# Kernel tuning notes

Measured on AMD Instinct MI355X. Metric: run time of the kernel, lower is better.

The kernel has to match this reference:

```python
import jax, jax.numpy as jnp
import numpy as np

B, S, D = 4, 8192, 512      # batch, seq_len, dim
P, M = 32, 2048             # num_persistent_memory, memory_size
EPS = 1e-5


def setup_inputs() -> dict:
    key = jax.random.key(0)
    ks = jax.random.split(key, 8)
    s = 1.0 / np.sqrt(D)

    def lin_w(k):
        return jax.random.uniform(k, (D, D), jnp.float32, -s, s)

    return {
        "x": jax.random.normal(ks[0], (B, S, D), jnp.float32),
        "persistent_memory": jax.random.normal(ks[1], (P, D), jnp.float32),
        "Wk": lin_w(ks[2]), "bk": jnp.zeros((D,), jnp.float32),
        "Wv": lin_w(ks[3]), "bv": jnp.zeros((D,), jnp.float32),
        "Wq": lin_w(ks[4]), "bq": jnp.zeros((D,), jnp.float32),
        "gamma": jnp.ones((D,), jnp.float32),
        "beta": jnp.zeros((D,), jnp.float32),
        "Wout": lin_w(ks[5]), "bout": jnp.zeros((D,), jnp.float32),
    }


def reference(x, persistent_memory, Wk, bk, Wv, bv, Wq, bq, gamma, beta, Wout, bout):
    b = x.shape[0]
    # concat persistent tokens: [B, T, D], T = P + S
    pm = jnp.broadcast_to(persistent_memory[None], (b, P, D))
    c = jnp.concatenate([pm, x], axis=1)

    k = c @ Wk + bk
    v = c @ Wv + bv
    q = c @ Wq + bq
    scale = 1.0 / jnp.sqrt(jnp.asarray(D, c.dtype))

    # init_state -> zeros [B, M, D]
    state0 = jnp.zeros((b, M, D), c.dtype)

    # update: write combined tokens into memory slots via cross-attention
    write_attn = jax.nn.softmax(jnp.einsum('bmd,btd->bmt', state0, k) * scale, axis=-1)  # [B,M,T]
    state = state0 + jnp.einsum('bmt,btd->bmd', write_attn, v)                           # [B,M,D]

    # retrieve: read memory with projected queries
    read_attn = jax.nn.softmax(jnp.einsum('btd,bmd->btm', q, state) * scale, axis=-1)    # [B,T,M]
    mem_out = jnp.einsum('btm,bmd->btd', read_attn, state)                               # [B,T,D]

    # LayerNorm
    mu = jnp.mean(mem_out, axis=-1, keepdims=True)
    var = jnp.mean((mem_out - mu) ** 2, axis=-1, keepdims=True)
    normed = (mem_out - mu) / jnp.sqrt(var + EPS) * gamma + beta

    # output projection (dropout is identity in eval mode)
    return normed @ Wout + bout
```

## Files before the change

kernel.cpp:

```cpp
#include <hip/hip_runtime.h>
#include <math.h>

#define BB 4
#define SS 8192
#define DD 512
#define PP 32
#define TT (PP + SS)
#define EPSV 1e-5f

typedef float f4 __attribute__((ext_vector_type(4)));


__global__ __launch_bounds__(512) void k_colsum(const f4* __restrict__ x4,
                                                f4* __restrict__ part4,
                                                float* __restrict__ z,
                                                const float* __restrict__ bout) {
  const int bb    = blockIdx.x >> 8;
  const int chunk = blockIdx.x & 255;
  const int tid   = threadIdx.x;

  const f4* p = x4 + ((size_t)bb * SS + (size_t)chunk * 32) * (DD / 4);

  f4 a = {0.f, 0.f, 0.f, 0.f};
#pragma unroll
  for (int i = 0; i < 8; ++i) {
    f4 t = __builtin_nontemporal_load(&p[i * 512 + tid]);
    a += t;
  }

  __shared__ f4 sh[512];
  sh[tid] = a;
  __syncthreads();

  if (tid < 128) {
    f4 r = sh[tid] + sh[tid + 128] + sh[tid + 256] + sh[tid + 384];
    part4[blockIdx.x * 128 + tid] = r;
  }

  if (blockIdx.x < BB) z[blockIdx.x * DD + tid] = bout[tid];
}

__global__ __launch_bounds__(512) void k_vbar(const float* __restrict__ part,
                                              const float* __restrict__ pm,
                                              const float* __restrict__ Wv,
                                              float* __restrict__ vpart) {
  const int bb = blockIdx.x >> 5;
  const int ch = blockIdx.x & 31;
  const int j  = threadIdx.x;

  __shared__ float aSh[16];
  {
    const int d16  = j >> 5;
    const int lane = j & 31;
    const int col  = ch * 16 + d16;
    float s0 = 0.f, s1 = 0.f;
#pragma unroll
    for (int k = 0; k < 4; ++k) {
      s0 += part[(size_t)(bb * 256 + lane + 64 * k) * DD + col];
      s1 += part[(size_t)(bb * 256 + lane + 64 * k + 32) * DD + col];
    }
    float s = s0 + s1 + pm[lane * DD + col];
#pragma unroll
    for (int off = 16; off > 0; off >>= 1) s += __shfl_down(s, off, 32);
    if (lane == 0) aSh[d16] = s * (1.0f / (float)TT);
  }
  __syncthreads();

  float acc = 0.f;
#pragma unroll
  for (int i = 0; i < 16; ++i)
    acc += aSh[i] * Wv[(ch * 16 + i) * DD + j];
  vpart[(bb * 32 + ch) * DD + j] = acc;
}

__global__ __launch_bounds__(512) void k_zmat(const float* __restrict__ vpart,
                                              const float* __restrict__ bv,
                                              const float* __restrict__ gamma,
                                              const float* __restrict__ beta,
                                              const float* __restrict__ Wout,
                                              float* __restrict__ z) {
  const int bb = blockIdx.x >> 5;
  const int ch = blockIdx.x & 31;
  const int j  = threadIdx.x;

  float va = bv[j], vb = 0.f;
#pragma unroll
  for (int c = 0; c < 16; ++c) {
    va += vpart[(bb * 32 + c) * DD + j];
    vb += vpart[(bb * 32 + c + 16) * DD + j];
  }
  const float v = va + vb;

  float v1 = v, v2 = v * v;
#pragma unroll
  for (int off = 32; off > 0; off >>= 1) {
    v1 += __shfl_down(v1, off, 64);
    v2 += __shfl_down(v2, off, 64);
  }
  __shared__ float w1[8], w2[8];
  const int wave = j >> 6;
  if ((j & 63) == 0) { w1[wave] = v1; w2[wave] = v2; }
  __syncthreads();
  float t1 = 0.f, t2 = 0.f;
#pragma unroll
  for (int w = 0; w < 8; ++w) { t1 += w1[w]; t2 += w2[w]; }
  const float mu  = t1 * (1.0f / (float)DD);
  const float var = t2 * (1.0f / (float)DD) - mu * mu;
  const float inv = 1.0f / sqrtf(var + EPSV);

  __shared__ float y[DD];
  y[j] = (v - mu) * inv * gamma[j] + beta[j];
  __syncthreads();

  float acc = 0.f;
#pragma unroll
  for (int i = 0; i < 16; ++i)
    acc += y[ch * 16 + i] * Wout[(ch * 16 + i) * DD + j];
  atomicAdd(&z[bb * DD + j], acc);
}

__global__ __launch_bounds__(256) void k_bcast(const f4* __restrict__ z4,
                                               f4* __restrict__ out4) {
  const unsigned i  = blockIdx.x * 256u + threadIdx.x;
  const unsigned bb = i / 1052672u;
  const unsigned j4 = i & 127u;
  __builtin_nontemporal_store(z4[bb * 128u + j4], &out4[i]);
}

extern "C" void kernel_launch(void* const* d_in, const int* in_sizes, int n_in,
                              void* d_out, int out_size, void* d_ws, size_t ws_size,
                              hipStream_t stream) {
  const float* x     = (const float*)d_in[0];
  const float* pm    = (const float*)d_in[1];
  const float* Wv    = (const float*)d_in[4];
  const float* bv    = (const float*)d_in[5];
  const float* gamma = (const float*)d_in[8];
  const float* beta  = (const float*)d_in[9];
  const float* Wout  = (const float*)d_in[10];
  const float* bout  = (const float*)d_in[11];

  float* part  = (float*)d_ws;
  float* vpart = part + 1024 * DD;
  float* z     = vpart + 128 * DD;

  k_colsum<<<1024, 512, 0, stream>>>((const f4*)x, (f4*)part, z, bout);

  k_vbar<<<BB * 32, 512, 0, stream>>>(part, pm, Wv, vpart);

  k_zmat<<<BB * 32, 512, 0, stream>>>(vpart, bv, gamma, beta, Wout, z);

  const unsigned total4 = (unsigned)BB * TT * DD / 4;
  k_bcast<<<total4 / 256, 256, 0, stream>>>((const f4*)z, (f4*)d_out);
}
```

Baseline: 144.1 us.

## Fuse vbar and zmat via algebraic LayerNorm split, shrink colsum grid

Merges the two middle kernels into one by rewriting LayerNorm-then-Wout algebraically: per-batch sum and sum-of-squares are accumulated with atomics, and the normalisation is applied in the broadcast kernel as inv*(v·gamma·Wout - mu·gamma·Wout) + beta·Wout + bout. The column-sum kernel now uses 256 larger blocks plus helper blocks that sum persistent memory and zero the accumulators. Nontemporal loads and stores are dropped. This removes one launch and its dependency, but makes the broadcast kernel compute per element, and the accumulators rely on atomics whose summation order is not fixed.

```diff
diff --git a/kernel.cpp b/kernel.cpp
--- a/kernel.cpp
+++ b/kernel.cpp
@@ -11,120 +11,146 @@
 typedef float f4 __attribute__((ext_vector_type(4)));
 
 
+#define OFF_PART  0
+#define OFF_PMSUM (256 * DD)
+#define OFF_AZ    (OFF_PMSUM + DD)
+#define OFF_G     (OFF_AZ + BB * DD)
+#define OFF_BZ    (OFF_G + DD)
+#define OFF_SV    (OFF_BZ + DD)
+#define OFF_SV2   (OFF_SV + BB * 16)
+
 __global__ __launch_bounds__(512) void k_colsum(const f4* __restrict__ x4,
-                                                f4* __restrict__ part4,
-                                                float* __restrict__ z,
-                                                const float* __restrict__ bout) {
-  const int bb    = blockIdx.x >> 8;
-  const int chunk = blockIdx.x & 255;
+                                                const float* __restrict__ pm,
+                                                const float* __restrict__ bout,
+                                                float* __restrict__ ws) {
+  const int tid = threadIdx.x;
+
+  if (blockIdx.x < 256) {
+    const int bb    = blockIdx.x >> 6;
+    const int chunk = blockIdx.x & 63;
+    const f4* p = x4 + ((size_t)bb * SS + (size_t)chunk * 128) * (DD / 4);
+
+    f4 a = {0.f, 0.f, 0.f, 0.f};
+#pragma unroll 8
+    for (int i = 0; i < 32; ++i)
+      a += p[i * 512 + tid];
+
+    __shared__ f4 sh[512];
+    sh[tid] = a;
+    __syncthreads();
+    if (tid < 128) {
+      f4 r = sh[tid] + sh[tid + 128] + sh[tid + 256] + sh[tid + 384];
+      ((f4*)(ws + OFF_PART))[blockIdx.x * 128 + tid] = r;
+    }
+  } else if (blockIdx.x == 256) {
+    float s = 0.f;
+#pragma unroll
+    for (int p = 0; p < PP; ++p) s += pm[p * DD + tid];
+    ws[OFF_PMSUM + tid] = s;
+  } else {
+#pragma unroll
+    for (int k = 0; k < BB; ++k) ws[OFF_AZ + k * DD + tid] = 0.f;
+    ws[OFF_G + tid]  = 0.f;
+    ws[OFF_BZ + tid] = bout[tid];
+    if (tid < BB) { ws[OFF_SV + tid * 16] = 0.f; ws[OFF_SV2 + tid * 16] = 0.f; }
+  }
+}
+
+__global__ __launch_bounds__(512) void k_mid(const float* __restrict__ Wv,
+                                             const float* __restrict__ bv,
+                                             const float* __restrict__ gamma,
+                                             const float* __restrict__ beta,
+                                             const float* __restrict__ Wout,
+                                             float* __restrict__ ws) {
+  const int bb    = blockIdx.x >> 5;
+  const int slice = blockIdx.x & 31;
   const int tid   = threadIdx.x;
 
-  const f4* p = x4 + ((size_t)bb * SS + (size_t)chunk * 32) * (DD / 4);
+  __shared__ float cbar[DD];
+  __shared__ float red[8][16];
+  __shared__ float vgSh[16];
 
-  f4 a = {0.f, 0.f, 0.f, 0.f};
-#pragma unroll
-  for (int i = 0; i < 8; ++i) {
-    f4 t = __builtin_nontemporal_load(&p[i * 512 + tid]);
-    a += t;
-  }
-
-  __shared__ f4 sh[512];
-  sh[tid] = a;
-  __syncthreads();
-
-  if (tid < 128) {
-    f4 r = sh[tid] + sh[tid + 128] + sh[tid + 256] + sh[tid + 384];
-    part4[blockIdx.x * 128 + tid] = r;
-  }
-
-  if (blockIdx.x < BB) z[blockIdx.x * DD + tid] = bout[tid];
-}
-
-__global__ __launch_bounds__(512) void k_vbar(const float* __restrict__ part,
-                                              const float* __restrict__ pm,
-                                              const float* __restrict__ Wv,
-                                              float* __restrict__ vpart) {
-  const int bb = blockIdx.x >> 5;
-  const int ch = blockIdx.x & 31;
-  const int j  = threadIdx.x;
-
-  __shared__ float aSh[16];
   {
-    const int d16  = j >> 5;
-    const int lane = j & 31;
-    const int col  = ch * 16 + d16;
+    const float* pb = ws + OFF_PART + (size_t)(bb * 64) * DD + tid;
     float s0 = 0.f, s1 = 0.f;
-#pragma unroll
-    for (int k = 0; k < 4; ++k) {
-      s0 += part[(size_t)(bb * 256 + lane + 64 * k) * DD + col];
-      s1 += part[(size_t)(bb * 256 + lane + 64 * k + 32) * DD + col];
+#pragma unroll 8
+    for (int r = 0; r < 32; ++r) {
+      s0 += pb[(size_t)(2 * r) * DD];
+      s1 += pb[(size_t)(2 * r + 1) * DD];
     }
-    float s = s0 + s1 + pm[lane * DD + col];
-#pragma unroll
-    for (int off = 16; off > 0; off >>= 1) s += __shfl_down(s, off, 32);
-    if (lane == 0) aSh[d16] = s * (1.0f / (float)TT);
+    cbar[tid] = (s0 + s1 + ws[OFF_PMSUM + tid]) * (1.0f / (float)TT);
   }
   __syncthreads();
 
-  float acc = 0.f;
+  const int c = tid & 15;
+  const int r = tid >> 4;
+  {
+    float acc = 0.f;
 #pragma unroll
-  for (int i = 0; i < 16; ++i)
-    acc += aSh[i] * Wv[(ch * 16 + i) * DD + j];
-  vpart[(bb * 32 + ch) * DD + j] = acc;
+    for (int i = 0; i < 16; ++i) {
+      const int k = r * 16 + i;
+      acc += cbar[k] * Wv[k * DD + slice * 16 + c];
+    }
+    acc += __shfl_xor(acc, 16, 64);
+    acc += __shfl_xor(acc, 32, 64);
+    if ((tid & 63) < 16) red[tid >> 6][c] = acc;
+  }
+  __syncthreads();
+
+  if (tid < 16) {
+    float v = bv[slice * 16 + tid];
+#pragma unroll
+    for (int w = 0; w < 8; ++w) v += red[w][tid];
+    red[0][tid] = v;
+    vgSh[tid]   = v * gamma[slice * 16 + tid];
+  }
+  __syncthreads();
+
+  if (tid == 0) {
+    float a = 0.f, q = 0.f;
+#pragma unroll
+    for (int t = 0; t < 16; ++t) { float vv = red[0][t]; a += vv; q += vv * vv; }
+    atomicAdd(ws + OFF_SV + bb * 16, a);
+    atomicAdd(ws + OFF_SV2 + bb * 16, q);
+  }
+
+  {
+    float acc = 0.f;
+#pragma unroll
+    for (int i = 0; i < 16; ++i)
+      acc += vgSh[i] * Wout[(slice * 16 + i) * DD + tid];
+    atomicAdd(ws + OFF_AZ + bb * DD + tid, acc);
+
+    if (bb == 1) {
+      float g = 0.f;
+#pragma unroll
+      for (int i = 0; i < 16; ++i)
+        g += gamma[slice * 16 + i] * Wout[(slice * 16 + i) * DD + tid];
+      atomicAdd(ws + OFF_G + tid, g);
+    } else if (bb == 2) {
+      float bz = 0.f;
+#pragma unroll
+      for (int i = 0; i < 16; ++i)
+        bz += beta[slice * 16 + i] * Wout[(slice * 16 + i) * DD + tid];
+      atomicAdd(ws + OFF_BZ + tid, bz);
+    }
+  }
 }
 
-__global__ __launch_bounds__(512) void k_zmat(const float* __restrict__ vpart,
-                                              const float* __restrict__ bv,
-                                              const float* __restrict__ gamma,
-                                              const float* __restrict__ beta,
-                                              const float* __restrict__ Wout,
-                                              float* __restrict__ z) {
-  const int bb = blockIdx.x >> 5;
-  const int ch = blockIdx.x & 31;
-  const int j  = threadIdx.x;
-
-  float va = bv[j], vb = 0.f;
-#pragma unroll
-  for (int c = 0; c < 16; ++c) {
-    va += vpart[(bb * 32 + c) * DD + j];
-    vb += vpart[(bb * 32 + c + 16) * DD + j];
-  }
-  const float v = va + vb;
-
-  float v1 = v, v2 = v * v;
-#pragma unroll
-  for (int off = 32; off > 0; off >>= 1) {
-    v1 += __shfl_down(v1, off, 64);
-    v2 += __shfl_down(v2, off, 64);
-  }
-  __shared__ float w1[8], w2[8];
-  const int wave = j >> 6;
-  if ((j & 63) == 0) { w1[wave] = v1; w2[wave] = v2; }
-  __syncthreads();
-  float t1 = 0.f, t2 = 0.f;
-#pragma unroll
-  for (int w = 0; w < 8; ++w) { t1 += w1[w]; t2 += w2[w]; }
-  const float mu  = t1 * (1.0f / (float)DD);
-  const float var = t2 * (1.0f / (float)DD) - mu * mu;
-  const float inv = 1.0f / sqrtf(var + EPSV);
-
-  __shared__ float y[DD];
-  y[j] = (v - mu) * inv * gamma[j] + beta[j];
-  __syncthreads();
-
-  float acc = 0.f;
-#pragma unroll
-  for (int i = 0; i < 16; ++i)
-    acc += y[ch * 16 + i] * Wout[(ch * 16 + i) * DD + j];
-  atomicAdd(&z[bb * DD + j], acc);
-}
-
-__global__ __launch_bounds__(256) void k_bcast(const f4* __restrict__ z4,
+__global__ __launch_bounds__(256) void k_bcast(const float* __restrict__ ws,
                                                f4* __restrict__ out4) {
   const unsigned i  = blockIdx.x * 256u + threadIdx.x;
   const unsigned bb = i / 1052672u;
   const unsigned j4 = i & 127u;
-  __builtin_nontemporal_store(z4[bb * 128u + j4], &out4[i]);
+
+  const float mu  = ws[OFF_SV + bb * 16] * (1.0f / (float)DD);
+  const float var = ws[OFF_SV2 + bb * 16] * (1.0f / (float)DD) - mu * mu;
+  const float inv = 1.0f / sqrtf(var + EPSV);
+
+  const f4 az = ((const f4*)(ws + OFF_AZ))[bb * 128u + j4];
+  const f4 g  = ((const f4*)(ws + OFF_G))[j4];
+  const f4 bz = ((const f4*)(ws + OFF_BZ))[j4];
+  out4[i] = inv * (az - mu * g) + bz;
 }
 
 extern "C" void kernel_launch(void* const* d_in, const int* in_sizes, int n_in,
@@ -139,16 +165,12 @@
   const float* Wout  = (const float*)d_in[10];
   const float* bout  = (const float*)d_in[11];
 
-  float* part  = (float*)d_ws;
-  float* vpart = part + 1024 * DD;
-  float* z     = vpart + 128 * DD;
+  float* ws = (float*)d_ws;
 
-  k_colsum<<<1024, 512, 0, stream>>>((const f4*)x, (f4*)part, z, bout);
+  k_colsum<<<258, 512, 0, stream>>>((const f4*)x, pm, bout, ws);
 
-  k_vbar<<<BB * 32, 512, 0, stream>>>(part, pm, Wv, vpart);
-
-  k_zmat<<<BB * 32, 512, 0, stream>>>(vpart, bv, gamma, beta, Wout, z);
+  k_mid<<<BB * 32, 512, 0, stream>>>(Wv, bv, gamma, beta, Wout, ws);
 
   const unsigned total4 = (unsigned)BB * TT * DD / 4;
-  k_bcast<<<total4 / 256, 256, 0, stream>>>((const f4*)z, (f4*)d_out);
+  k_bcast<<<total4 / 256, 256, 0, stream>>>(ws, (f4*)d_out);
 }
```

Result: no change. 143.3 us (-0.6%).
